# Kernel optimization log

Hardware: AMD Instinct MI355X
Metric: run time of the kernel (lower is better)

The kernel has to match this reference:

```python
import jax, jax.numpy as jnp
import numpy as np

DIM = 4096
N_HEAD = 32
N_KV_HEAD = 8
HEAD_DIM = DIM // N_HEAD  # 128
B, T = 2, 2048


def _rope_freqs(T, head_dim, theta=10000.0):
    inv = 1.0 / (theta ** (np.arange(0, head_dim, 2, dtype=np.float32) / head_dim))
    t = np.arange(T, dtype=np.float32)
    ang = np.outer(t, inv)  # [T, head_dim/2]
    return jnp.asarray(np.stack([np.cos(ang), np.sin(ang)], axis=-1))  # [T, hd/2, 2]


def setup_inputs() -> dict:
    key = jax.random.key(0)
    ks = jax.random.split(key, 5)
    s = 1.0 / np.sqrt(DIM)
    return {
        "x": jax.random.normal(ks[0], (B, T, DIM), dtype=jnp.float32),
        "freqs_cis": _rope_freqs(T, HEAD_DIM),
        "wq": jax.random.normal(ks[1], (DIM, N_HEAD * HEAD_DIM), dtype=jnp.float32) * s,
        "wk": jax.random.normal(ks[2], (DIM, N_KV_HEAD * HEAD_DIM), dtype=jnp.float32) * s,
        "wv": jax.random.normal(ks[3], (DIM, N_KV_HEAD * HEAD_DIM), dtype=jnp.float32) * s,
        "wo": jax.random.normal(ks[4], (DIM, DIM), dtype=jnp.float32) * s,
    }


def _apply_rotary(x, freqs_cis):
    # x: [B, T, H, head_dim]; freqs_cis: [T, head_dim/2, 2]
    xs = x.reshape(*x.shape[:-1], -1, 2)  # [B, T, H, hd/2, 2]
    fc = freqs_cis[None, :, None, :, :]   # [1, T, 1, hd/2, 2]
    real = xs[..., 0] * fc[..., 0] - xs[..., 1] * fc[..., 1]
    imag = xs[..., 1] * fc[..., 0] + xs[..., 0] * fc[..., 1]
    return jnp.stack([real, imag], axis=-1).reshape(x.shape)


def reference(x, freqs_cis, wq, wk, wv, wo):
    Bx, Tx, C = x.shape
    q = (x @ wq).reshape(Bx, Tx, N_HEAD, HEAD_DIM)
    k = (x @ wk).reshape(Bx, Tx, N_KV_HEAD, HEAD_DIM)
    v = (x @ wv).reshape(Bx, Tx, N_KV_HEAD, HEAD_DIM)
    q = _apply_rotary(q, freqs_cis)
    k = _apply_rotary(k, freqs_cis)
    # [B, H, T, hd]
    q = q.transpose(0, 2, 1, 3)
    k = k.transpose(0, 2, 1, 3)
    v = v.transpose(0, 2, 1, 3)
    # GQA: expand kv heads to match query heads
    rep = N_HEAD // N_KV_HEAD
    k = jnp.repeat(k, rep, axis=1)
    v = jnp.repeat(v, rep, axis=1)
    scale = 1.0 / np.sqrt(HEAD_DIM)
    scores = jnp.einsum("bhqd,bhkd->bhqk", q, k) * scale
    causal = jnp.tril(jnp.ones((Tx, Tx), dtype=bool))
    scores = jnp.where(causal[None, None], scores, jnp.float32(-1e30))
    attn = jax.nn.softmax(scores, axis=-1)
    y = jnp.einsum("bhqk,bhkd->bhqd", attn, v)
    y = y.transpose(0, 2, 1, 3).reshape(Bx, Tx, C)
    return y @ wo
```

## Files before the change

### kernel.cpp

```cpp
#include <hip/hip_runtime.h>

#define DIM  4096
#define NH   32
#define NKV  8
#define HD   128
#define BSZ  2
#define TSEQ 2048

typedef __bf16 bf16x8 __attribute__((ext_vector_type(8)));
typedef unsigned short ushort8v __attribute__((ext_vector_type(8)));
typedef float f32x4 __attribute__((ext_vector_type(4)));

typedef void GV __attribute__((address_space(1)));
typedef void LV __attribute__((address_space(3)));

__device__ __forceinline__ unsigned short f2bf(float f) {
  unsigned u = __builtin_bit_cast(unsigned, f);
  u += 0x7FFFu + ((u >> 16) & 1u);
  return (unsigned short)(u >> 16);
}
__device__ __forceinline__ float bf2f(unsigned short b) {
  unsigned u = ((unsigned)b) << 16;
  return __builtin_bit_cast(float, u);
}
__device__ __forceinline__ void gload16(const unsigned short* g, unsigned short* l) {
  __builtin_amdgcn_global_load_lds((GV*)g, (LV*)l, 16, 0, 0);
}
__device__ __forceinline__ f32x4 mfma16(bf16x8 a, bf16x8 b, f32x4 c) {
  return __builtin_amdgcn_mfma_f32_16x16x32_bf16(a, b, c, 0, 0, 0);
}
__device__ __forceinline__ bf16x8 lds8(const unsigned short* p) {
  return __builtin_bit_cast(bf16x8, *(const ushort8v*)p);
}

__global__ void detect_dtype(const unsigned int* __restrict__ fc, int* __restrict__ flag) {
  if (threadIdx.x == 0 && blockIdx.x == 0)
    *flag = (fc[0] == 0x3F800000u) ? 0 : 1;
}

__global__ void cast_x(const void* __restrict__ src, unsigned short* __restrict__ dst,
                       const int* __restrict__ flag) {
  long t = (long)blockIdx.x * 256 + threadIdx.x;
  if (*flag) {
    ((uint2*)dst)[t] = ((const uint2*)src)[t];
  } else {
    float4 f = ((const float4*)src)[t];
    ushort4 o;
    o.x = f2bf(f.x); o.y = f2bf(f.y); o.z = f2bf(f.z); o.w = f2bf(f.w);
    ((ushort4*)dst)[t] = o;
  }
}

__global__ __launch_bounds__(256) void transpose64(const void* __restrict__ src,
                                                   unsigned short* __restrict__ dst,
                                                   int R, int C, const int* __restrict__ flag) {
  __shared__ unsigned short tile[64][68];
  const int isbf = *flag;
  const int tid = threadIdx.x;
  const int c0g = blockIdx.x * 64, r0g = blockIdx.y * 64;
  const int cc = (tid & 15) * 4;
  if (isbf) {
    const unsigned short* s = (const unsigned short*)src;
#pragma unroll
    for (int it = 0; it < 4; ++it) {
      const int r = it * 16 + (tid >> 4);
      ushort4 v = *(const ushort4*)(s + (long)(r0g + r) * C + c0g + cc);
      *(ushort4*)&tile[r][cc] = v;
    }
  } else {
    const float* s = (const float*)src;
#pragma unroll
    for (int it = 0; it < 4; ++it) {
      const int r = it * 16 + (tid >> 4);
      float4 f = *(const float4*)(s + (long)(r0g + r) * C + c0g + cc);
      ushort4 v;
      v.x = f2bf(f.x); v.y = f2bf(f.y); v.z = f2bf(f.z); v.w = f2bf(f.w);
      *(ushort4*)&tile[r][cc] = v;
    }
  }
  __syncthreads();
#pragma unroll
  for (int it = 0; it < 2; ++it) {
    const int c = (tid >> 3) + it * 32;
    const int r0 = (tid & 7) * 8;
    ushort8v o;
#pragma unroll
    for (int u = 0; u < 8; ++u) o[u] = tile[r0 + u][c];
    *(ushort8v*)(dst + (long)(c0g + c) * R + r0g + r0) = o;
  }
}

__device__ __forceinline__ void gemm128_loop(const unsigned short* __restrict__ A,
                                             const unsigned short* __restrict__ Bt,
                                             unsigned short* As, unsigned short* Bs,
                                             long tileM, long tileN, f32x4 (&acc)[4][4]) {
  const int tid = (int)threadIdx.x;
  const int lane = tid & 63, wave = tid >> 6;
  const int wr = wave >> 1, wc = wave & 1;
  const int lm = lane & 15, quad = lane >> 4;
  const int sr = tid >> 3;
  const int schunk = ((tid & 7) ^ (sr & 7)) * 8;
  const unsigned short* Ag = A + (tileM + sr) * 4096L + schunk;
  const unsigned short* Bg = Bt + (tileN + sr) * 4096L + schunk;
  unsigned short* Al = As + sr * 64 + (tid & 7) * 8;
  unsigned short* Bl = Bs + sr * 64 + (tid & 7) * 8;

  auto stgA = [&](int slot, int half, int tt) {
    const unsigned short* g = Ag + (long)half * (64 * 4096L) + (long)tt * 64;
    unsigned short* l = Al + slot * 8192 + half * 4096;
    gload16(g, l);
    gload16(g + 32 * 4096L, l + 2048);
  };
  auto stgB = [&](int slot, int half, int tt) {
    const unsigned short* g = Bg + (long)half * (64 * 4096L) + (long)tt * 64;
    unsigned short* l = Bl + slot * 8192 + half * 4096;
    gload16(g, l);
    gload16(g + 32 * 4096L, l + 2048);
  };
  auto rdA = [&](int so, int f, int kk) {
    return lds8(&As[so + (wr * 64 + f * 16 + lm) * 64 + (((kk * 4 + quad) ^ (lm & 7)) * 8)]);
  };
  auto rdB = [&](int so, int f, int kk) {
    return lds8(&Bs[so + (wc * 64 + f * 16 + lm) * 64 + (((kk * 4 + quad) ^ (lm & 7)) * 8)]);
  };

  stgB(0, 0, 0); stgB(0, 1, 0); stgA(0, 0, 0); stgA(0, 1, 0);
  stgB(1, 0, 1); stgB(1, 1, 1); stgA(1, 0, 1);
  asm volatile("s_waitcnt vmcnt(6)" ::: "memory");
  __builtin_amdgcn_sched_barrier(0);
  __builtin_amdgcn_s_barrier();

#pragma unroll 2
  for (int t = 0; t < 64; ++t) {
    __builtin_amdgcn_sched_barrier(0);
    const int s = t & 1;
    const int so = s * 8192;
    bf16x8 a[4][2], b[4][2];
#pragma unroll
    for (int f = 0; f < 4; ++f) { a[f][0] = rdA(so, f, 0); a[f][1] = rdA(so, f, 1); }
#pragma unroll
    for (int f = 0; f < 4; ++f) { b[f][0] = rdB(so, f, 0); b[f][1] = rdB(so, f, 1); }
    if (t < 63) stgA(s ^ 1, 1, t + 1);
    __builtin_amdgcn_sched_barrier(0);
    __builtin_amdgcn_s_barrier();
    asm volatile("s_waitcnt lgkmcnt(0)" ::: "memory");
    __builtin_amdgcn_sched_barrier(0);
    __builtin_amdgcn_s_setprio(1);
#pragma unroll
    for (int mf = 0; mf < 4; ++mf)
#pragma unroll
      for (int nf = 0; nf < 2; ++nf)
        acc[mf][nf] = mfma16(a[mf][0], b[nf][0], acc[mf][nf]);
    __builtin_amdgcn_s_setprio(0);
    __builtin_amdgcn_sched_barrier(0);
    __builtin_amdgcn_s_barrier();
    if (t < 62) stgB(s, 0, t + 2);
    __builtin_amdgcn_sched_barrier(0);
    __builtin_amdgcn_s_barrier();
    __builtin_amdgcn_sched_barrier(0);
    __builtin_amdgcn_s_setprio(1);
#pragma unroll
    for (int mf = 0; mf < 4; ++mf)
#pragma unroll
      for (int nf = 0; nf < 2; ++nf)
        acc[mf][nf + 2] = mfma16(a[mf][0], b[nf + 2][0], acc[mf][nf + 2]);
    __builtin_amdgcn_s_setprio(0);
    __builtin_amdgcn_sched_barrier(0);
    __builtin_amdgcn_s_barrier();
    if (t < 62) stgB(s, 1, t + 2);
    __builtin_amdgcn_sched_barrier(0);
    __builtin_amdgcn_s_barrier();
    __builtin_amdgcn_sched_barrier(0);
    __builtin_amdgcn_s_setprio(1);
#pragma unroll
    for (int mf = 0; mf < 4; ++mf)
#pragma unroll
      for (int nf = 0; nf < 2; ++nf)
        acc[mf][nf] = mfma16(a[mf][1], b[nf][1], acc[mf][nf]);
    __builtin_amdgcn_s_setprio(0);
    __builtin_amdgcn_sched_barrier(0);
    __builtin_amdgcn_s_barrier();
    if (t < 62) stgA(s, 0, t + 2);
    __builtin_amdgcn_sched_barrier(0);
    __builtin_amdgcn_s_barrier();
    __builtin_amdgcn_sched_barrier(0);
    __builtin_amdgcn_s_setprio(1);
#pragma unroll
    for (int mf = 0; mf < 4; ++mf)
#pragma unroll
      for (int nf = 0; nf < 2; ++nf)
        acc[mf][nf + 2] = mfma16(a[mf][1], b[nf + 2][1], acc[mf][nf + 2]);
    __builtin_amdgcn_s_setprio(0);
    if (t < 62)       asm volatile("s_waitcnt vmcnt(6)" ::: "memory");
    else if (t == 62) asm volatile("s_waitcnt vmcnt(0)" ::: "memory");
    __builtin_amdgcn_sched_barrier(0);
    __builtin_amdgcn_s_barrier();
  }
}

__global__ __launch_bounds__(256, 2) void gemm_qkv8(const unsigned short* __restrict__ A,
                                                    const unsigned short* __restrict__ Bt,
                                                    const void* __restrict__ fcv,
                                                    const int* __restrict__ flag,
                                                    unsigned short* __restrict__ qo,
                                                    unsigned short* __restrict__ ko,
                                                    unsigned short* __restrict__ vo) {
  __shared__ __align__(16) unsigned short As[2 * 8192];
  __shared__ __align__(16) unsigned short Bs[2 * 8192];
  const int bid = (int)blockIdx.x;
  const int nb2 = (bid & 7) * 192 + (bid >> 3);
  const long tileM = (long)(nb2 / 48) * 128;
  const long tileN = (long)(nb2 % 48) * 128;
  f32x4 acc[4][4] = {};
  gemm128_loop(A, Bt, As, Bs, tileM, tileN, acc);
  const int tid = (int)threadIdx.x;
  const int lane = tid & 63, wave = tid >> 6;
  const int wr = wave >> 1, wc = wave & 1;
  const int lm = lane & 15, quad = lane >> 4;
  const int isbf = *flag;
  const int nb = (int)tileN + wc * 64;
  if (nb < 5120) {
    const int isk = (nb >= 4096);
    unsigned short* dst = isk ? ko : qo;
    const int hpb = isk ? NKV : NH;
    const int coff = isk ? 4096 : 0;
#pragma unroll
    for (int mf = 0; mf < 4; ++mf)
#pragma unroll
      for (int r = 0; r < 4; ++r) {
        const int m = (int)tileM + wr * 64 + mf * 16 + quad * 4 + r;
        const int b = m >> 11, tq = m & (TSEQ - 1);
#pragma unroll
        for (int nf = 0; nf < 4; ++nf) {
          const int n = nb + nf * 16 + lm;
          float val = acc[mf][nf][r];
          float par = __shfl_xor(val, 1);
          const int ip = (n & 127) >> 1;
          const long fo = (long)tq * 64 + ip;
          float cz, sz;
          if (isbf) {
            const unsigned short* fu = (const unsigned short*)fcv;
            cz = bf2f(fu[fo * 2]); sz = bf2f(fu[fo * 2 + 1]);
          } else {
            float2 cs = ((const float2*)fcv)[fo];
            cz = cs.x; sz = cs.y;
          }
          float out = (n & 1) ? (val * cz + par * sz) : (val * cz - par * sz);
          const int h = (n - coff) >> 7, d = n & 127;
          dst[((long)(b * hpb + h) * TSEQ + tq) * HD + d] = f2bf(out);
        }
      }
  } else {
#pragma unroll
    for (int mf = 0; mf < 4; ++mf)
#pragma unroll
      for (int r = 0; r < 4; ++r) {
        const int m = (int)tileM + wr * 64 + mf * 16 + quad * 4 + r;
        const int b = m >> 11, tq = m & (TSEQ - 1);
#pragma unroll
        for (int nf = 0; nf < 4; ++nf) {
          const int n = nb + nf * 16 + lm;
          const int h = (n - 5120) >> 7, d = n & 127;
          vo[((long)(b * NKV + h) * HD + d) * TSEQ + tq] = f2bf(acc[mf][nf][r]);
        }
      }
  }
}

__global__ __launch_bounds__(256, 2) void gemm_wo8(const unsigned short* __restrict__ A,
                                                   const unsigned short* __restrict__ Bt,
                                                   void* __restrict__ Cv,
                                                   const int* __restrict__ flag) {
  __shared__ __align__(16) unsigned short As[2 * 8192];
  __shared__ __align__(16) unsigned short Bs[2 * 8192];
  const int bid = (int)blockIdx.x;
  const int nb2 = (bid & 7) * 128 + (bid >> 3);
  const long tileM = (long)(nb2 >> 5) * 128;
  const long tileN = (long)(nb2 & 31) * 128;
  f32x4 acc[4][4] = {};
  gemm128_loop(A, Bt, As, Bs, tileM, tileN, acc);
  const int tid = (int)threadIdx.x;
  const int lane = tid & 63, wave = tid >> 6;
  const int wr = wave >> 1, wc = wave & 1;
  const int lm = lane & 15, quad = lane >> 4;
  const int obf = *flag;
  const long N = 4096;
  if (obf) {
    unsigned short* C = (unsigned short*)Cv;
#pragma unroll
    for (int mf = 0; mf < 4; ++mf)
#pragma unroll
      for (int nf = 0; nf < 4; ++nf)
#pragma unroll
        for (int r = 0; r < 4; ++r)
          C[(tileM + wr * 64 + mf * 16 + quad * 4 + r) * N + tileN + wc * 64 + nf * 16 + lm] =
              f2bf(acc[mf][nf][r]);
  } else {
    float* C = (float*)Cv;
#pragma unroll
    for (int mf = 0; mf < 4; ++mf)
#pragma unroll
      for (int nf = 0; nf < 4; ++nf)
#pragma unroll
        for (int r = 0; r < 4; ++r)
          C[(tileM + wr * 64 + mf * 16 + quad * 4 + r) * N + tileN + wc * 64 + nf * 16 + lm] =
              acc[mf][nf][r];
  }
}

__global__ __launch_bounds__(256, 3) void flash_attn(const unsigned short* __restrict__ q,
                                                     const unsigned short* __restrict__ k,
                                                     const unsigned short* __restrict__ vT,
                                                     unsigned short* __restrict__ y) {
  __shared__ unsigned short Ks[2][32 * 128];
  __shared__ unsigned short Vs[2][128 * 32];
  __shared__ unsigned short Pl[4][32 * 40];
  const int tid = threadIdx.x;
  const int lane = tid & 63, wave = tid >> 6;
  const int lm = lane & 15, quad = lane >> 4;
  const int bh = blockIdx.y, b = bh >> 5, h = bh & 31, kvh = h >> 2;
  const int qi = (int)gridDim.x - 1 - (int)blockIdx.x;
  const int q0 = qi * 128;
  const unsigned short* Qb = q + ((long)(b * NH + h) * TSEQ + q0 + wave * 32) * HD;
  const unsigned short* Kb = k + (long)(b * NKV + kvh) * TSEQ * HD;
  const unsigned short* Vb = vT + (long)(b * NKV + kvh) * HD * TSEQ;
  bf16x8 qf[2][4];
#pragma unroll
  for (int mi = 0; mi < 2; ++mi)
#pragma unroll
    for (int ks = 0; ks < 4; ++ks)
      qf[mi][ks] = __builtin_bit_cast(bf16x8,
          *(const ushort8v*)(Qb + (mi * 16 + lm) * HD + ks * 32 + quad * 8));
  f32x4 o[2][8] = {};
  float li[2][4] = {};
  const float scale = 0.08838834764831845f;
  const int krow = tid >> 4, kcl = ((tid & 15) ^ (krow & 7)) * 8;
  const int vrow = tid >> 2, vcl = ((tid & 3) ^ ((vrow >> 1) & 3)) * 8;
  const int ktiles = qi * 4 + 4;
  {
    gload16(Kb + krow * HD + kcl, &Ks[0][tid * 8]);
    gload16(Kb + (16 + krow) * HD + kcl, &Ks[0][2048 + tid * 8]);
    gload16(Vb + (long)vrow * TSEQ + vcl, &Vs[0][tid * 8]);
    gload16(Vb + (long)(64 + vrow) * TSEQ + vcl, &Vs[0][2048 + tid * 8]);
  }
  for (int kt = 0; kt < ktiles; ++kt) {
    __syncthreads();
    if (kt + 1 < ktiles) {
      const int bi = (kt + 1) & 1;
      const unsigned short* Kg = Kb + (long)(kt + 1) * 32 * HD;
      gload16(Kg + krow * HD + kcl, &Ks[bi][tid * 8]);
      gload16(Kg + (16 + krow) * HD + kcl, &Ks[bi][2048 + tid * 8]);
      const unsigned short* Vg = Vb + (kt + 1) * 32;
      gload16(Vg + (long)vrow * TSEQ + vcl, &Vs[bi][tid * 8]);
      gload16(Vg + (long)(64 + vrow) * TSEQ + vcl, &Vs[bi][2048 + tid * 8]);
    }
    const unsigned short* KsB = Ks[kt & 1];
    const unsigned short* VsB = Vs[kt & 1];
    f32x4 s[2][2] = {};
#pragma unroll
    for (int ni = 0; ni < 2; ++ni)
#pragma unroll
      for (int ks = 0; ks < 4; ++ks) {
        bf16x8 kf = lds8(&KsB[(ni * 16 + lm) * 128 + ((ks * 4 + quad) ^ (lm & 7)) * 8]);
        s[0][ni] = mfma16(qf[0][ks], kf, s[0][ni]);
        s[1][ni] = mfma16(qf[1][ks], kf, s[1][ni]);
      }
    unsigned short* PlW = &Pl[wave][0];
#pragma unroll
    for (int mi = 0; mi < 2; ++mi)
#pragma unroll
      for (int r = 0; r < 4; ++r) {
        const int qg = q0 + wave * 32 + mi * 16 + quad * 4 + r;
#pragma unroll
        for (int ni = 0; ni < 2; ++ni) {
          const int kg = kt * 32 + ni * 16 + lm;
          float p = (kg <= qg) ? __expf(s[mi][ni][r] * scale) : 0.f;
          li[mi][r] += p;
          PlW[(mi * 16 + quad * 4 + r) * 40 + ni * 16 + lm] = f2bf(p);
        }
      }
    bf16x8 pf0 = lds8(&PlW[lm * 40 + quad * 8]);
    bf16x8 pf1 = lds8(&PlW[(16 + lm) * 40 + quad * 8]);
#pragma unroll
    for (int db = 0; db < 8; ++db) {
      bf16x8 vf = lds8(&VsB[(db * 16 + lm) * 32 + (quad ^ ((lm >> 1) & 3)) * 8]);
      o[0][db] = mfma16(pf0, vf, o[0][db]);
      o[1][db] = mfma16(pf1, vf, o[1][db]);
    }
  }
  float inv[2][4];
#pragma unroll
  for (int mi = 0; mi < 2; ++mi)
#pragma unroll
    for (int r = 0; r < 4; ++r) {
      float l = li[mi][r];
      l += __shfl_xor(l, 1, 16);
      l += __shfl_xor(l, 2, 16);
      l += __shfl_xor(l, 4, 16);
      l += __shfl_xor(l, 8, 16);
      inv[mi][r] = 1.0f / l;
    }
  unsigned short* yo = y + ((long)b * TSEQ + q0 + wave * 32) * DIM + h * 128 + lm;
#pragma unroll
  for (int mi = 0; mi < 2; ++mi)
#pragma unroll
    for (int r = 0; r < 4; ++r) {
      unsigned short* yr = yo + (long)(mi * 16 + quad * 4 + r) * DIM;
#pragma unroll
      for (int db = 0; db < 8; ++db)
        yr[db * 16] = f2bf(o[mi][db][r] * inv[mi][r]);
    }
}

extern "C" void kernel_launch(void* const* d_in, const int* in_sizes, int n_in,
                              void* d_out, int out_size, void* d_ws, size_t ws_size,
                              hipStream_t stream) {
  const void* x  = d_in[0];
  const void* fc = d_in[1];
  const void* wq = d_in[2];
  const void* wk = d_in[3];
  const void* wv = d_in[4];
  const void* wo = d_in[5];
  char* ws = (char*)d_ws;
  int* flag             = (int*)ws;
  unsigned short* xb    = (unsigned short*)(ws + 256);
  unsigned short* wqkvT = xb + 16777216L;
  unsigned short* woT   = wqkvT + 25165824L;
  unsigned short* qb    = woT + 16777216L;
  unsigned short* kb    = qb + 16777216L;
  unsigned short* vb    = kb + 4194304L;
  unsigned short* yb    = xb;

  detect_dtype<<<dim3(1), dim3(64), 0, stream>>>((const unsigned int*)fc, flag);
  cast_x<<<dim3(16384), dim3(256), 0, stream>>>(x, xb, flag);
  transpose64<<<dim3(64, 64), dim3(256), 0, stream>>>(wq, wqkvT, 4096, 4096, flag);
  transpose64<<<dim3(16, 64), dim3(256), 0, stream>>>(wk, wqkvT + 4096L * 4096, 4096, 1024, flag);
  transpose64<<<dim3(16, 64), dim3(256), 0, stream>>>(wv, wqkvT + 5120L * 4096, 4096, 1024, flag);
  transpose64<<<dim3(64, 64), dim3(256), 0, stream>>>(wo, woT, 4096, 4096, flag);
  gemm_qkv8<<<dim3(1536), dim3(256), 0, stream>>>(xb, wqkvT, fc, flag, qb, kb, vb);
  flash_attn<<<dim3(16, 64), dim3(256), 0, stream>>>(qb, kb, vb, yb);
  gemm_wo8<<<dim3(1024), dim3(256), 0, stream>>>(yb, woT, d_out, flag);
}
```

Before: 846.3 us.

## Pair causal attention q-tiles per block and merge GEMM pipeline phases

```diff
diff --git a/kernel.cpp b/kernel.cpp
--- a/kernel.cpp
+++ b/kernel.cpp
@@ -141,55 +141,24 @@
 #pragma unroll
     for (int f = 0; f < 4; ++f) { b[f][0] = rdB(so, f, 0); b[f][1] = rdB(so, f, 1); }
     if (t < 63) stgA(s ^ 1, 1, t + 1);
-    __builtin_amdgcn_sched_barrier(0);
-    __builtin_amdgcn_s_barrier();
     asm volatile("s_waitcnt lgkmcnt(0)" ::: "memory");
     __builtin_amdgcn_sched_barrier(0);
     __builtin_amdgcn_s_setprio(1);
 #pragma unroll
     for (int mf = 0; mf < 4; ++mf)
 #pragma unroll
-      for (int nf = 0; nf < 2; ++nf)
+      for (int nf = 0; nf < 4; ++nf)
         acc[mf][nf] = mfma16(a[mf][0], b[nf][0], acc[mf][nf]);
     __builtin_amdgcn_s_setprio(0);
     __builtin_amdgcn_sched_barrier(0);
     __builtin_amdgcn_s_barrier();
-    if (t < 62) stgB(s, 0, t + 2);
-    __builtin_amdgcn_sched_barrier(0);
-    __builtin_amdgcn_s_barrier();
-    __builtin_amdgcn_sched_barrier(0);
+    if (t < 62) { stgB(s, 0, t + 2); stgB(s, 1, t + 2); stgA(s, 0, t + 2); }
     __builtin_amdgcn_s_setprio(1);
 #pragma unroll
     for (int mf = 0; mf < 4; ++mf)
 #pragma unroll
-      for (int nf = 0; nf < 2; ++nf)
-        acc[mf][nf + 2] = mfma16(a[mf][0], b[nf + 2][0], acc[mf][nf + 2]);
-    __builtin_amdgcn_s_setprio(0);
-    __builtin_amdgcn_sched_barrier(0);
-    __builtin_amdgcn_s_barrier();
-    if (t < 62) stgB(s, 1, t + 2);
-    __builtin_amdgcn_sched_barrier(0);
-    __builtin_amdgcn_s_barrier();
-    __builtin_amdgcn_sched_barrier(0);
-    __builtin_amdgcn_s_setprio(1);
-#pragma unroll
-    for (int mf = 0; mf < 4; ++mf)
-#pragma unroll
-      for (int nf = 0; nf < 2; ++nf)
+      for (int nf = 0; nf < 4; ++nf)
         acc[mf][nf] = mfma16(a[mf][1], b[nf][1], acc[mf][nf]);
-    __builtin_amdgcn_s_setprio(0);
-    __builtin_amdgcn_sched_barrier(0);
-    __builtin_amdgcn_s_barrier();
-    if (t < 62) stgA(s, 0, t + 2);
-    __builtin_amdgcn_sched_barrier(0);
-    __builtin_amdgcn_s_barrier();
-    __builtin_amdgcn_sched_barrier(0);
-    __builtin_amdgcn_s_setprio(1);
-#pragma unroll
-    for (int mf = 0; mf < 4; ++mf)
-#pragma unroll
-      for (int nf = 0; nf < 2; ++nf)
-        acc[mf][nf + 2] = mfma16(a[mf][1], b[nf + 2][1], acc[mf][nf + 2]);
     __builtin_amdgcn_s_setprio(0);
     if (t < 62)       asm volatile("s_waitcnt vmcnt(6)" ::: "memory");
     else if (t == 62) asm volatile("s_waitcnt vmcnt(0)" ::: "memory");
@@ -319,97 +288,102 @@
   const int lane = tid & 63, wave = tid >> 6;
   const int lm = lane & 15, quad = lane >> 4;
   const int bh = blockIdx.y, b = bh >> 5, h = bh & 31, kvh = h >> 2;
-  const int qi = (int)gridDim.x - 1 - (int)blockIdx.x;
-  const int q0 = qi * 128;
-  const unsigned short* Qb = q + ((long)(b * NH + h) * TSEQ + q0 + wave * 32) * HD;
+  const int pr = (int)blockIdx.x;
   const unsigned short* Kb = k + (long)(b * NKV + kvh) * TSEQ * HD;
   const unsigned short* Vb = vT + (long)(b * NKV + kvh) * HD * TSEQ;
-  bf16x8 qf[2][4];
-#pragma unroll
-  for (int mi = 0; mi < 2; ++mi)
-#pragma unroll
-    for (int ks = 0; ks < 4; ++ks)
-      qf[mi][ks] = __builtin_bit_cast(bf16x8,
-          *(const ushort8v*)(Qb + (mi * 16 + lm) * HD + ks * 32 + quad * 8));
-  f32x4 o[2][8] = {};
-  float li[2][4] = {};
   const float scale = 0.08838834764831845f;
   const int krow = tid >> 4, kcl = ((tid & 15) ^ (krow & 7)) * 8;
   const int vrow = tid >> 2, vcl = ((tid & 3) ^ ((vrow >> 1) & 3)) * 8;
-  const int ktiles = qi * 4 + 4;
-  {
-    gload16(Kb + krow * HD + kcl, &Ks[0][tid * 8]);
-    gload16(Kb + (16 + krow) * HD + kcl, &Ks[0][2048 + tid * 8]);
-    gload16(Vb + (long)vrow * TSEQ + vcl, &Vs[0][tid * 8]);
-    gload16(Vb + (long)(64 + vrow) * TSEQ + vcl, &Vs[0][2048 + tid * 8]);
-  }
-  for (int kt = 0; kt < ktiles; ++kt) {
-    __syncthreads();
-    if (kt + 1 < ktiles) {
-      const int bi = (kt + 1) & 1;
-      const unsigned short* Kg = Kb + (long)(kt + 1) * 32 * HD;
-      gload16(Kg + krow * HD + kcl, &Ks[bi][tid * 8]);
-      gload16(Kg + (16 + krow) * HD + kcl, &Ks[bi][2048 + tid * 8]);
-      const unsigned short* Vg = Vb + (kt + 1) * 32;
-      gload16(Vg + (long)vrow * TSEQ + vcl, &Vs[bi][tid * 8]);
-      gload16(Vg + (long)(64 + vrow) * TSEQ + vcl, &Vs[bi][2048 + tid * 8]);
+
+  for (int seg = 0; seg < 2; ++seg) {
+    const int qi = seg ? (15 - pr) : pr;
+    const int q0 = qi * 128;
+    const unsigned short* Qb = q + ((long)(b * NH + h) * TSEQ + q0 + wave * 32) * HD;
+    bf16x8 qf[2][4];
+#pragma unroll
+    for (int mi = 0; mi < 2; ++mi)
+#pragma unroll
+      for (int ks = 0; ks < 4; ++ks)
+        qf[mi][ks] = __builtin_bit_cast(bf16x8,
+            *(const ushort8v*)(Qb + (mi * 16 + lm) * HD + ks * 32 + quad * 8));
+    f32x4 o[2][8] = {};
+    float li[2][4] = {};
+    const int ktiles = qi * 4 + 4;
+    if (seg) __syncthreads();
+    {
+      gload16(Kb + krow * HD + kcl, &Ks[0][tid * 8]);
+      gload16(Kb + (16 + krow) * HD + kcl, &Ks[0][2048 + tid * 8]);
+      gload16(Vb + (long)vrow * TSEQ + vcl, &Vs[0][tid * 8]);
+      gload16(Vb + (long)(64 + vrow) * TSEQ + vcl, &Vs[0][2048 + tid * 8]);
     }
-    const unsigned short* KsB = Ks[kt & 1];
-    const unsigned short* VsB = Vs[kt & 1];
-    f32x4 s[2][2] = {};
-#pragma unroll
-    for (int ni = 0; ni < 2; ++ni)
-#pragma unroll
-      for (int ks = 0; ks < 4; ++ks) {
-        bf16x8 kf = lds8(&KsB[(ni * 16 + lm) * 128 + ((ks * 4 + quad) ^ (lm & 7)) * 8]);
-        s[0][ni] = mfma16(qf[0][ks], kf, s[0][ni]);
-        s[1][ni] = mfma16(qf[1][ks], kf, s[1][ni]);
-      }
-    unsigned short* PlW = &Pl[wave][0];
+    for (int kt = 0; kt < ktiles; ++kt) {
+      __syncthreads();
+      if (kt + 1 < ktiles) {
+        const int bi = (kt + 1) & 1;
+        const unsigned short* Kg = Kb + (long)(kt + 1) * 32 * HD;
+        gload16(Kg + krow * HD + kcl, &Ks[bi][tid * 8]);
+        gload16(Kg + (16 + krow) * HD + kcl, &Ks[bi][2048 + tid * 8]);
+        const unsigned short* Vg = Vb + (kt + 1) * 32;
+        gload16(Vg + (long)vrow * TSEQ + vcl, &Vs[bi][tid * 8]);
+        gload16(Vg + (long)(64 + vrow) * TSEQ + vcl, &Vs[bi][2048 + tid * 8]);
+      }
+      const unsigned short* KsB = Ks[kt & 1];
+      const unsigned short* VsB = Vs[kt & 1];
+      f32x4 s[2][2] = {};
+#pragma unroll
+      for (int ni = 0; ni < 2; ++ni)
+#pragma unroll
+        for (int ks = 0; ks < 4; ++ks) {
+          bf16x8 kf = lds8(&KsB[(ni * 16 + lm) * 128 + ((ks * 4 + quad) ^ (lm & 7)) * 8]);
+          s[0][ni] = mfma16(qf[0][ks], kf, s[0][ni]);
+          s[1][ni] = mfma16(qf[1][ks], kf, s[1][ni]);
+        }
+      unsigned short* PlW = &Pl[wave][0];
+#pragma unroll
+      for (int mi = 0; mi < 2; ++mi)
+#pragma unroll
+        for (int r = 0; r < 4; ++r) {
+          const int qg = q0 + wave * 32 + mi * 16 + quad * 4 + r;
+#pragma unroll
+          for (int ni = 0; ni < 2; ++ni) {
+            const int kg = kt * 32 + ni * 16 + lm;
+            float p = (kg <= qg) ? __expf(s[mi][ni][r] * scale) : 0.f;
+            li[mi][r] += p;
+            PlW[(mi * 16 + quad * 4 + r) * 40 + ni * 16 + lm] = f2bf(p);
+          }
+        }
+      bf16x8 pf0 = lds8(&PlW[lm * 40 + quad * 8]);
+      bf16x8 pf1 = lds8(&PlW[(16 + lm) * 40 + quad * 8]);
+#pragma unroll
+      for (int db = 0; db < 8; ++db) {
+        bf16x8 vf = lds8(&VsB[(db * 16 + lm) * 32 + (quad ^ ((lm >> 1) & 3)) * 8]);
+        o[0][db] = mfma16(pf0, vf, o[0][db]);
+        o[1][db] = mfma16(pf1, vf, o[1][db]);
+      }
+    }
+    float inv[2][4];
 #pragma unroll
     for (int mi = 0; mi < 2; ++mi)
 #pragma unroll
       for (int r = 0; r < 4; ++r) {
-        const int qg = q0 + wave * 32 + mi * 16 + quad * 4 + r;
-#pragma unroll
-        for (int ni = 0; ni < 2; ++ni) {
-          const int kg = kt * 32 + ni * 16 + lm;
-          float p = (kg <= qg) ? __expf(s[mi][ni][r] * scale) : 0.f;
-          li[mi][r] += p;
-          PlW[(mi * 16 + quad * 4 + r) * 40 + ni * 16 + lm] = f2bf(p);
-        }
-      }
-    bf16x8 pf0 = lds8(&PlW[lm * 40 + quad * 8]);
-    bf16x8 pf1 = lds8(&PlW[(16 + lm) * 40 + quad * 8]);
-#pragma unroll
-    for (int db = 0; db < 8; ++db) {
-      bf16x8 vf = lds8(&VsB[(db * 16 + lm) * 32 + (quad ^ ((lm >> 1) & 3)) * 8]);
-      o[0][db] = mfma16(pf0, vf, o[0][db]);
-      o[1][db] = mfma16(pf1, vf, o[1][db]);
-    }
-  }
-  float inv[2][4];
-#pragma unroll
-  for (int mi = 0; mi < 2; ++mi)
-#pragma unroll
-    for (int r = 0; r < 4; ++r) {
-      float l = li[mi][r];
-      l += __shfl_xor(l, 1, 16);
-      l += __shfl_xor(l, 2, 16);
-      l += __shfl_xor(l, 4, 16);
-      l += __shfl_xor(l, 8, 16);
-      inv[mi][r] = 1.0f / l;
-    }
-  unsigned short* yo = y + ((long)b * TSEQ + q0 + wave * 32) * DIM + h * 128 + lm;
-#pragma unroll
-  for (int mi = 0; mi < 2; ++mi)
-#pragma unroll
-    for (int r = 0; r < 4; ++r) {
-      unsigned short* yr = yo + (long)(mi * 16 + quad * 4 + r) * DIM;
-#pragma unroll
-      for (int db = 0; db < 8; ++db)
-        yr[db * 16] = f2bf(o[mi][db][r] * inv[mi][r]);
-    }
+        float l = li[mi][r];
+        l += __shfl_xor(l, 1, 16);
+        l += __shfl_xor(l, 2, 16);
+        l += __shfl_xor(l, 4, 16);
+        l += __shfl_xor(l, 8, 16);
+        inv[mi][r] = 1.0f / l;
+      }
+    unsigned short* yo = y + ((long)b * TSEQ + q0 + wave * 32) * DIM + h * 128 + lm;
+#pragma unroll
+    for (int mi = 0; mi < 2; ++mi)
+#pragma unroll
+      for (int r = 0; r < 4; ++r) {
+        unsigned short* yr = yo + (long)(mi * 16 + quad * 4 + r) * DIM;
+#pragma unroll
+        for (int db = 0; db < 8; ++db)
+          yr[db * 16] = f2bf(o[mi][db][r] * inv[mi][r]);
+      }
+  }
 }
 
 extern "C" void kernel_launch(void* const* d_in, const int* in_sizes, int n_in,
@@ -438,6 +412,6 @@
   transpose64<<<dim3(16, 64), dim3(256), 0, stream>>>(wv, wqkvT + 5120L * 4096, 4096, 1024, flag);
   transpose64<<<dim3(64, 64), dim3(256), 0, stream>>>(wo, woT, 4096, 4096, flag);
   gemm_qkv8<<<dim3(1536), dim3(256), 0, stream>>>(xb, wqkvT, fc, flag, qb, kb, vb);
-  flash_attn<<<dim3(16, 64), dim3(256), 0, stream>>>(qb, kb, vb, yb);
+  flash_attn<<<dim3(8, 64), dim3(256), 0, stream>>>(qb, kb, vb, yb);
   gemm_wo8<<<dim3(1024), dim3(256), 0, stream>>>(yb, woT, d_out, flag);
 }
```

Measured after the change: 773.9 us. 1.09x faster.
